# Performance work log

Hardware: AMD Instinct MI355X
Metric: run time of the kernel (lower is better)

The kernel has to match this reference:

```python
import jax, jax.numpy as jnp
import numpy as np

B, NAG = 8192, 16          # scenes, agents per scene
CIN, CH = 64, 128          # gnn_in_channels, gnn_out_channels
R2 = 8.0 * 8.0             # comm_range squared
BOX = 20.0                 # positions sampled uniformly in [0, BOX]^2


def _lin(k, fi, fo):
    k1, k2 = jax.random.split(k)
    s = 1.0 / np.sqrt(fi)
    W = jax.random.uniform(k1, (fi, fo), jnp.float32, -s, s)
    b = jax.random.uniform(k2, (fo,), jnp.float32, -s, s)
    return W, b


def setup_inputs() -> dict:
    key = jax.random.key(0)
    ks = jax.random.split(key, 10)
    x = jax.random.normal(ks[0], (B * NAG, CIN), jnp.float32)          # VAE mu per agent
    pos = jax.random.uniform(ks[1], (B, NAG, 2), jnp.float32) * BOX    # sensor xy positions
    W_rel1, b_rel1 = _lin(ks[2], CIN, CH)
    W_root1, _ = _lin(ks[3], CIN, CH)
    W_rel2, b_rel2 = _lin(ks[4], CH, CH)
    W_root2, _ = _lin(ks[5], CH, CH)
    Wh1, bh1 = _lin(ks[6], 2 * CH, 64)
    Wh2, bh2 = _lin(ks[7], 64, 32)
    Wh3, bh3 = _lin(ks[8], 32, 16)
    return dict(x=x, pos=pos, W_rel1=W_rel1, b_rel1=b_rel1, W_root1=W_root1,
                W_rel2=W_rel2, b_rel2=b_rel2, W_root2=W_root2,
                Wh1=Wh1, bh1=bh1, Wh2=Wh2, bh2=bh2, Wh3=Wh3, bh3=bh3)


def _graph_conv(h, adj, W_rel, b_rel, W_root):
    # PyG GraphConv (aggr='add'): out_i = W_rel @ sum_{j in N(i)} h_j + b_rel + W_root @ h_i
    nb = adj.shape[0]
    hb = h.reshape(nb, NAG, h.shape[-1])                 # [B, n, C]
    agg = jnp.einsum('bij,bjc->bic', adj, hb)            # neighbor sum within each scene
    return agg.reshape(h.shape[0], -1) @ W_rel + b_rel + h @ W_root


def reference(x, pos, W_rel1, b_rel1, W_root1, W_rel2, b_rel2, W_root2,
              Wh1, bh1, Wh2, bh2, Wh3, bh3):
    # radius_graph (batch-isolated, loop=False) as a per-scene dense mask
    diff = pos[:, :, None, :] - pos[:, None, :, :]       # [B, n, n, 2]
    d2 = jnp.sum(diff * diff, axis=-1)                   # [B, n, n]
    eye = jnp.eye(NAG, dtype=bool)
    adj = ((d2 <= R2) & ~eye).astype(x.dtype)            # [B, n, n]
    # Dropout(p=0.2) omitted (eval / deterministic reference).
    x1 = jax.nn.relu(_graph_conv(x, adj, W_rel1, b_rel1, W_root1))   # named 'x1' (inplace ReLU)
    x2 = jax.nn.relu(_graph_conv(x1, adj, W_rel2, b_rel2, W_root2))  # named 'x2' (inplace ReLU)
    h = jnp.concatenate([x1, x2], axis=-1)               # JumpingKnowledge('cat')
    h = jax.nn.relu(h @ Wh1 + bh1)
    h = jax.nn.relu(h @ Wh2 + bh2)
    out = h @ Wh3 + bh3                                  # [N, 16]
    return out.reshape(B, NAG, 16)
```

## Files before the change

### kernel.cpp

```cpp
#include <hip/hip_runtime.h>

#define NAG 16
#define SPB 4
#define NBLK 2048
#define R2f 64.0f

typedef unsigned short u16;
typedef __attribute__((ext_vector_type(8))) short short8;
typedef __attribute__((ext_vector_type(4))) float f32x4;

#define MFMA(a, b, c) __builtin_amdgcn_mfma_f32_16x16x32_bf16(a, b, c, 0, 0, 0)

#define OFF_B1 0
#define OFF_B2 16384
#define OFF_H1 49152
#define OFF_H2 65536
#define OFF_H3 67584
#define SWZ_UNITS 8512

__device__ __forceinline__ u16 f2b(float f) {
    unsigned u = __float_as_uint(f);
    unsigned r = u + 0x7FFFu + ((u >> 16) & 1u);
    return (u16)(r >> 16);
}

__global__ __launch_bounds__(256) void swizzle_w(
    const float* __restrict__ Wrel1, const float* __restrict__ Wroot1,
    const float* __restrict__ Wrel2, const float* __restrict__ Wroot2,
    const float* __restrict__ Wh1,  const float* __restrict__ Wh2,
    const float* __restrict__ Wh3,  u16* __restrict__ ws)
{
    const int u = blockIdx.x * 256 + threadIdx.x;
    if (u >= SWZ_UNITS) return;

    int v, T, N, ksplit;
    const float *W, *W2;
    u16* dst;
    if (u < 2048)      { v = u;        T = 8; N = 128; ksplit = 64;  W = Wroot1; W2 = Wrel1; dst = ws + OFF_B1 + v * 8; }
    else if (u < 6144) { v = u - 2048; T = 8; N = 128; ksplit = 128; W = Wroot2; W2 = Wrel2; dst = ws + OFF_B2 + v * 8; }
    else if (u < 8192) { v = u - 6144; T = 4; N = 64;  ksplit = 1 << 30; W = Wh1; W2 = Wh1; dst = ws + OFF_H1 + v * 8; }
    else if (u < 8448) { v = u - 8192; T = 2; N = 32;  ksplit = 1 << 30; W = Wh2; W2 = Wh2; dst = ws + OFF_H2 + v * 8; }
    else               { v = u - 8448; T = 1; N = 16;  ksplit = 1 << 30; W = Wh3; W2 = Wh3; dst = ws + OFF_H3 + v * 8; }

    const int lane = v & 63;
    const int t = (v >> 6) % T;
    const int s = (v >> 6) / T;
    const int n = t * 16 + (lane & 15);
    const int k0 = s * 32 + (lane >> 4) * 8;
    #pragma unroll
    for (int j = 0; j < 8; ++j) {
        const int k = k0 + j;
        const float val = (k < ksplit) ? W[k * N + n] : W2[(k - ksplit) * N + n];
        dst[j] = f2b(val);
    }
}

__device__ __forceinline__ short8 ldfrag(const u16* __restrict__ ws, int off,
                                         int T, int s, int tile, int lane) {
    return *(const short8*)(ws + off + (size_t)(((s * T + tile) * 64 + lane) * 8));
}

__device__ __forceinline__ short8 make_adjA(unsigned m, int q, int odd) {
    union { short8 v; unsigned u[4]; } r;
    const bool on = (q >> 1) == odd;
    const int base = (q & 1) * 8;
    #pragma unroll
    for (int jj = 0; jj < 4; ++jj) {
        const int k0 = base + 2 * jj;
        const unsigned lo = (on && ((m >> k0) & 1u)) ? 0x3F80u : 0u;
        const unsigned hi = (on && ((m >> (k0 + 1)) & 1u)) ? 0x3F80u : 0u;
        r.u[jj] = lo | (hi << 16);
    }
    return r.v;
}

__device__ __forceinline__ void relu_store4(u16* d, f32x4 a) {
    const unsigned p0 = (unsigned)f2b(fmaxf(a[0], 0.f)) | ((unsigned)f2b(fmaxf(a[1], 0.f)) << 16);
    const unsigned p1 = (unsigned)f2b(fmaxf(a[2], 0.f)) | ((unsigned)f2b(fmaxf(a[3], 0.f)) << 16);
    uint2 u; u.x = p0; u.y = p1;
    *(uint2*)d = u;
}

__global__ __launch_bounds__(256) void gnn_fused4(
    const float* __restrict__ x, const float* __restrict__ pos,
    const float* __restrict__ brel1, const float* __restrict__ brel2,
    const float* __restrict__ bh1,  const float* __restrict__ bh2,
    const float* __restrict__ bh3,
    const u16* __restrict__ ws, float* __restrict__ out)
{
    __shared__ __align__(16) u16 pool[39424];
    __shared__ unsigned mask[64];
    u16* const xcat = pool;
    u16* const xT   = pool + 8704;
    u16* const xc2  = pool + 13312;
    u16* const x1T  = pool + 30208;
    u16* const x2b  = pool;
    u16* const h1b  = pool + 8704;
    u16* const h2b  = pool + 30208;

    const int t = threadIdx.x;
    const int wv = t >> 6, lane = t & 63, ln = lane & 15, q = lane >> 4;
    const size_t sA = (size_t)blockIdx.x * SPB;

    {
        const int r = t >> 2;
        const int co = (t & 3) * 16;
        const float* src = x + (sA * 16 + r) * 64 + co;
        const float4 v0 = *(const float4*)(src);
        const float4 v1 = *(const float4*)(src + 4);
        const float4 v2 = *(const float4*)(src + 8);
        const float4 v3 = *(const float4*)(src + 12);
        u16 h[16];
        h[0] = f2b(v0.x); h[1] = f2b(v0.y); h[2]  = f2b(v0.z); h[3]  = f2b(v0.w);
        h[4] = f2b(v1.x); h[5] = f2b(v1.y); h[6]  = f2b(v1.z); h[7]  = f2b(v1.w);
        h[8] = f2b(v2.x); h[9] = f2b(v2.y); h[10] = f2b(v2.z); h[11] = f2b(v2.w);
        h[12]= f2b(v3.x); h[13]= f2b(v3.y); h[14] = f2b(v3.z); h[15] = f2b(v3.w);
        uint4 ua, ub;
        ua.x = (unsigned)h[0]  | ((unsigned)h[1]  << 16);
        ua.y = (unsigned)h[2]  | ((unsigned)h[3]  << 16);
        ua.z = (unsigned)h[4]  | ((unsigned)h[5]  << 16);
        ua.w = (unsigned)h[6]  | ((unsigned)h[7]  << 16);
        ub.x = (unsigned)h[8]  | ((unsigned)h[9]  << 16);
        ub.y = (unsigned)h[10] | ((unsigned)h[11] << 16);
        ub.z = (unsigned)h[12] | ((unsigned)h[13] << 16);
        ub.w = (unsigned)h[14] | ((unsigned)h[15] << 16);
        *(uint4*)&xcat[r * 136 + co]     = ua;
        *(uint4*)&xcat[r * 136 + co + 8] = ub;
        #pragma unroll
        for (int i = 0; i < 16; ++i)
            xT[(co + i) * 72 + r] = h[i];
    }
    if (t < 64) {
        const int g = t >> 4, a = t & 15;
        const float* pp = pos + (sA + g) * (NAG * 2);
        const float ax = pp[2 * a], ay = pp[2 * a + 1];
        unsigned m = 0;
        for (int j = 0; j < NAG; ++j) {
            const float dx = ax - pp[2 * j], dy = ay - pp[2 * j + 1];
            if (dx * dx + dy * dy <= R2f && j != a) m |= (1u << j);
        }
        mask[g * 16 + a] = m;
    }
    __syncthreads();

    {
        const int nt = wv;
        const short8 B0 = *(const short8*)&xT[(nt * 16 + ln) * 72 + q * 8];
        const short8 B1 = *(const short8*)&xT[(nt * 16 + ln) * 72 + 32 + q * 8];
        #pragma unroll
        for (int g = 0; g < 4; ++g) {
            const short8 A = make_adjA(mask[g * 16 + ln], q, g & 1);
            f32x4 acc = {0.f, 0.f, 0.f, 0.f};
            acc = MFMA(A, (g < 2) ? B0 : B1, acc);
            #pragma unroll
            for (int r = 0; r < 4; ++r)
                xcat[(g * 16 + q * 4 + r) * 136 + 64 + nt * 16 + ln] = f2b(acc[r]);
        }
    }
    __syncthreads();

    {
        const int n0 = 2 * wv, n1 = 2 * wv + 1;
        short8 Bf0[4], Bf1[4];
        #pragma unroll
        for (int s = 0; s < 4; ++s) {
            Bf0[s] = ldfrag(ws, OFF_B1, 8, s, n0, lane);
            Bf1[s] = ldfrag(ws, OFF_B1, 8, s, n1, lane);
        }
        const float b0 = brel1[n0 * 16 + ln], b1 = brel1[n1 * 16 + ln];
        #pragma unroll
        for (int m = 0; m < 4; ++m) {
            short8 Af[4];
            #pragma unroll
            for (int s = 0; s < 4; ++s)
                Af[s] = *(const short8*)&xcat[(m * 16 + ln) * 136 + s * 32 + q * 8];
            f32x4 a0 = {b0, b0, b0, b0}, a1 = {b1, b1, b1, b1};
            #pragma unroll
            for (int s = 0; s < 4; ++s) {
                a0 = MFMA(Af[s], Bf0[s], a0);
                a1 = MFMA(Af[s], Bf1[s], a1);
            }
            #pragma unroll
            for (int r = 0; r < 4; ++r) {
                const int row = m * 16 + q * 4 + r;
                xc2[row * 264 + n0 * 16 + ln] = f2b(fmaxf(a0[r], 0.f));
                xc2[row * 264 + n1 * 16 + ln] = f2b(fmaxf(a1[r], 0.f));
            }
            relu_store4(&x1T[(n0 * 16 + ln) * 72 + m * 16 + q * 4], a0);
            relu_store4(&x1T[(n1 * 16 + ln) * 72 + m * 16 + q * 4], a1);
        }
    }
    __syncthreads();

    {
        const int n0 = 2 * wv, n1 = 2 * wv + 1;
        short8 B00 = *(const short8*)&x1T[(n0 * 16 + ln) * 72 + q * 8];
        short8 B01 = *(const short8*)&x1T[(n0 * 16 + ln) * 72 + 32 + q * 8];
        short8 B10 = *(const short8*)&x1T[(n1 * 16 + ln) * 72 + q * 8];
        short8 B11 = *(const short8*)&x1T[(n1 * 16 + ln) * 72 + 32 + q * 8];
        #pragma unroll
        for (int g = 0; g < 4; ++g) {
            const short8 A = make_adjA(mask[g * 16 + ln], q, g & 1);
            f32x4 a0 = {0.f, 0.f, 0.f, 0.f}, a1 = a0;
            a0 = MFMA(A, (g < 2) ? B00 : B01, a0);
            a1 = MFMA(A, (g < 2) ? B10 : B11, a1);
            #pragma unroll
            for (int r = 0; r < 4; ++r) {
                const int row = g * 16 + q * 4 + r;
                xc2[row * 264 + 128 + n0 * 16 + ln] = f2b(a0[r]);
                xc2[row * 264 + 128 + n1 * 16 + ln] = f2b(a1[r]);
            }
        }
    }
    __syncthreads();

    {
        const int n0 = 2 * wv, n1 = 2 * wv + 1;
        short8 Bf0[8], Bf1[8];
        #pragma unroll
        for (int s = 0; s < 8; ++s) {
            Bf0[s] = ldfrag(ws, OFF_B2, 8, s, n0, lane);
            Bf1[s] = ldfrag(ws, OFF_B2, 8, s, n1, lane);
        }
        const float b0 = brel2[n0 * 16 + ln], b1 = brel2[n1 * 16 + ln];
        #pragma unroll
        for (int m = 0; m < 4; ++m) {
            short8 Af[8];
            #pragma unroll
            for (int s = 0; s < 8; ++s)
                Af[s] = *(const short8*)&xc2[(m * 16 + ln) * 264 + s * 32 + q * 8];
            f32x4 a0 = {b0, b0, b0, b0}, a1 = {b1, b1, b1, b1};
            f32x4 c0 = {0.f, 0.f, 0.f, 0.f}, c1 = c0;
            #pragma unroll
            for (int s = 0; s < 4; ++s) {
                a0 = MFMA(Af[s], Bf0[s], a0);
                a1 = MFMA(Af[s], Bf1[s], a1);
                c0 = MFMA(Af[s + 4], Bf0[s + 4], c0);
                c1 = MFMA(Af[s + 4], Bf1[s + 4], c1);
            }
            #pragma unroll
            for (int r = 0; r < 4; ++r) {
                const int row = m * 16 + q * 4 + r;
                x2b[row * 136 + n0 * 16 + ln] = f2b(fmaxf(a0[r] + c0[r], 0.f));
                x2b[row * 136 + n1 * 16 + ln] = f2b(fmaxf(a1[r] + c1[r], 0.f));
            }
        }
    }
    __syncthreads();

    {
        const int nt = wv;
        short8 Bf[8];
        #pragma unroll
        for (int s = 0; s < 8; ++s)
            Bf[s] = ldfrag(ws, OFF_H1, 4, s, nt, lane);
        const float b = bh1[nt * 16 + ln];
        #pragma unroll
        for (int m = 0; m < 4; ++m) {
            short8 Af[8];
            #pragma unroll
            for (int s = 0; s < 4; ++s)
                Af[s] = *(const short8*)&xc2[(m * 16 + ln) * 264 + s * 32 + q * 8];
            #pragma unroll
            for (int s = 0; s < 4; ++s)
                Af[s + 4] = *(const short8*)&x2b[(m * 16 + ln) * 136 + s * 32 + q * 8];
            f32x4 a = {b, b, b, b}, c = {0.f, 0.f, 0.f, 0.f};
            #pragma unroll
            for (int s = 0; s < 4; ++s) {
                a = MFMA(Af[s], Bf[s], a);
                c = MFMA(Af[s + 4], Bf[s + 4], c);
            }
            #pragma unroll
            for (int r = 0; r < 4; ++r)
                h1b[(m * 16 + q * 4 + r) * 72 + nt * 16 + ln] = f2b(fmaxf(a[r] + c[r], 0.f));
        }
    }
    __syncthreads();

    {
        const int nt = wv & 1;
        const int m0 = (wv >> 1) * 2;
        short8 Bf[2];
        Bf[0] = ldfrag(ws, OFF_H2, 2, 0, nt, lane);
        Bf[1] = ldfrag(ws, OFF_H2, 2, 1, nt, lane);
        const float b = bh2[nt * 16 + ln];
        #pragma unroll
        for (int mi = 0; mi < 2; ++mi) {
            const int m = m0 + mi;
            const short8 A0 = *(const short8*)&h1b[(m * 16 + ln) * 72 + q * 8];
            const short8 A1 = *(const short8*)&h1b[(m * 16 + ln) * 72 + 32 + q * 8];
            f32x4 a = {b, b, b, b};
            a = MFMA(A0, Bf[0], a);
            a = MFMA(A1, Bf[1], a);
            #pragma unroll
            for (int r = 0; r < 4; ++r)
                h2b[(m * 16 + q * 4 + r) * 40 + nt * 16 + ln] = f2b(fmaxf(a[r], 0.f));
        }
    }
    __syncthreads();

    {
        const int m = wv;
        const short8 A = *(const short8*)&h2b[(m * 16 + ln) * 40 + q * 8];
        const short8 B = ldfrag(ws, OFF_H3, 1, 0, 0, lane);
        const float b = bh3[ln];
        f32x4 a = {b, b, b, b};
        a = MFMA(A, B, a);
        float* o = out + (sA * 16 + m * 16) * 16;
        #pragma unroll
        for (int r = 0; r < 4; ++r)
            o[(q * 4 + r) * 16 + ln] = a[r];
    }
}

extern "C" void kernel_launch(void* const* d_in, const int* in_sizes, int n_in,
                              void* d_out, int out_size, void* d_ws, size_t ws_size,
                              hipStream_t stream) {
    const float* x      = (const float*)d_in[0];
    const float* pos    = (const float*)d_in[1];
    const float* Wrel1  = (const float*)d_in[2];
    const float* brel1  = (const float*)d_in[3];
    const float* Wroot1 = (const float*)d_in[4];
    const float* Wrel2  = (const float*)d_in[5];
    const float* brel2  = (const float*)d_in[6];
    const float* Wroot2 = (const float*)d_in[7];
    const float* Wh1    = (const float*)d_in[8];
    const float* bh1    = (const float*)d_in[9];
    const float* Wh2    = (const float*)d_in[10];
    const float* bh2    = (const float*)d_in[11];
    const float* Wh3    = (const float*)d_in[12];
    const float* bh3    = (const float*)d_in[13];
    u16* ws = (u16*)d_ws;

    swizzle_w<<<(SWZ_UNITS + 255) / 256, 256, 0, stream>>>(
        Wrel1, Wroot1, Wrel2, Wroot2, Wh1, Wh2, Wh3, ws);
    gnn_fused4<<<NBLK, 256, 0, stream>>>(
        x, pos, brel1, brel2, bh1, bh2, bh3, ws, (float*)d_out);
}
```

Measured before the change: 135.6 us.

## Reassociate GraphConv as adj@(h@W_rel) and shrink shared memory footprint

Each GraphConv layer now computes h@W_rel first, stores the result transposed in LDS, and then applies the adjacency MFMA to that projected result. The root term and the bias are accumulated into the same accumulator. This drops the separate aggregation pass, the concatenated xcat/xc2 buffers and one barrier, and the last two head layers are merged into one stage, so LDS use falls from about 79KB to about 53KB, which may raise occupancy. It also replaces round-to-nearest-even bf16 conversion with a cheaper round-half-up, which can change results slightly, and the adjacency fragments are built once and reused by both layers.

```diff
diff --git a/kernel.cpp b/kernel.cpp
--- a/kernel.cpp
+++ b/kernel.cpp
@@ -22,6 +22,13 @@
     unsigned u = __float_as_uint(f);
     unsigned r = u + 0x7FFFu + ((u >> 16) & 1u);
     return (u16)(r >> 16);
+}
+__device__ __forceinline__ unsigned rb(float f) {
+    return (__float_as_uint(f) + 0x8000u) >> 16;
+}
+__device__ __forceinline__ unsigned pk2(float a, float b) {
+    return ((__float_as_uint(a) + 0x8000u) >> 16) |
+           ((__float_as_uint(b) + 0x8000u) & 0xFFFF0000u);
 }
 
 __global__ __launch_bounds__(256) void swizzle_w(
@@ -32,7 +39,6 @@
 {
     const int u = blockIdx.x * 256 + threadIdx.x;
     if (u >= SWZ_UNITS) return;
-
     int v, T, N, ksplit;
     const float *W, *W2;
     u16* dst;
@@ -41,7 +47,6 @@
     else if (u < 8192) { v = u - 6144; T = 4; N = 64;  ksplit = 1 << 30; W = Wh1; W2 = Wh1; dst = ws + OFF_H1 + v * 8; }
     else if (u < 8448) { v = u - 8192; T = 2; N = 32;  ksplit = 1 << 30; W = Wh2; W2 = Wh2; dst = ws + OFF_H2 + v * 8; }
     else               { v = u - 8448; T = 1; N = 16;  ksplit = 1 << 30; W = Wh3; W2 = Wh3; dst = ws + OFF_H3 + v * 8; }
-
     const int lane = v & 63;
     const int t = (v >> 6) % T;
     const int s = (v >> 6) / T;
@@ -74,61 +79,39 @@
     return r.v;
 }
 
-__device__ __forceinline__ void relu_store4(u16* d, f32x4 a) {
-    const unsigned p0 = (unsigned)f2b(fmaxf(a[0], 0.f)) | ((unsigned)f2b(fmaxf(a[1], 0.f)) << 16);
-    const unsigned p1 = (unsigned)f2b(fmaxf(a[2], 0.f)) | ((unsigned)f2b(fmaxf(a[3], 0.f)) << 16);
-    uint2 u; u.x = p0; u.y = p1;
-    *(uint2*)d = u;
-}
-
-__global__ __launch_bounds__(256) void gnn_fused4(
+__global__ __launch_bounds__(256) void gnn_fused5(
     const float* __restrict__ x, const float* __restrict__ pos,
     const float* __restrict__ brel1, const float* __restrict__ brel2,
     const float* __restrict__ bh1,  const float* __restrict__ bh2,
     const float* __restrict__ bh3,
     const u16* __restrict__ ws, float* __restrict__ out)
 {
-    __shared__ __align__(16) u16 pool[39424];
+    __shared__ __align__(16) u16 pool[26624];
     __shared__ unsigned mask[64];
-    u16* const xcat = pool;
-    u16* const xT   = pool + 8704;
-    u16* const xc2  = pool + 13312;
-    u16* const x1T  = pool + 30208;
-    u16* const x2b  = pool;
-    u16* const h1b  = pool + 8704;
-    u16* const h2b  = pool + 30208;
+    u16* const xb  = pool;
+    u16* const yT  = pool + 8704;
+    u16* const x1b = pool + 17920;
 
     const int t = threadIdx.x;
     const int wv = t >> 6, lane = t & 63, ln = lane & 15, q = lane >> 4;
+    const int c0 = 32 * wv;
+    const int n0 = 2 * wv, n1 = 2 * wv + 1;
     const size_t sA = (size_t)blockIdx.x * SPB;
 
     {
-        const int r = t >> 2;
-        const int co = (t & 3) * 16;
+        const int r = t >> 2, co = (t & 3) * 16;
         const float* src = x + (sA * 16 + r) * 64 + co;
         const float4 v0 = *(const float4*)(src);
         const float4 v1 = *(const float4*)(src + 4);
         const float4 v2 = *(const float4*)(src + 8);
         const float4 v3 = *(const float4*)(src + 12);
-        u16 h[16];
-        h[0] = f2b(v0.x); h[1] = f2b(v0.y); h[2]  = f2b(v0.z); h[3]  = f2b(v0.w);
-        h[4] = f2b(v1.x); h[5] = f2b(v1.y); h[6]  = f2b(v1.z); h[7]  = f2b(v1.w);
-        h[8] = f2b(v2.x); h[9] = f2b(v2.y); h[10] = f2b(v2.z); h[11] = f2b(v2.w);
-        h[12]= f2b(v3.x); h[13]= f2b(v3.y); h[14] = f2b(v3.z); h[15] = f2b(v3.w);
         uint4 ua, ub;
-        ua.x = (unsigned)h[0]  | ((unsigned)h[1]  << 16);
-        ua.y = (unsigned)h[2]  | ((unsigned)h[3]  << 16);
-        ua.z = (unsigned)h[4]  | ((unsigned)h[5]  << 16);
-        ua.w = (unsigned)h[6]  | ((unsigned)h[7]  << 16);
-        ub.x = (unsigned)h[8]  | ((unsigned)h[9]  << 16);
-        ub.y = (unsigned)h[10] | ((unsigned)h[11] << 16);
-        ub.z = (unsigned)h[12] | ((unsigned)h[13] << 16);
-        ub.w = (unsigned)h[14] | ((unsigned)h[15] << 16);
-        *(uint4*)&xcat[r * 136 + co]     = ua;
-        *(uint4*)&xcat[r * 136 + co + 8] = ub;
-        #pragma unroll
-        for (int i = 0; i < 16; ++i)
-            xT[(co + i) * 72 + r] = h[i];
+        ua.x = pk2(v0.x, v0.y); ua.y = pk2(v0.z, v0.w);
+        ua.z = pk2(v1.x, v1.y); ua.w = pk2(v1.z, v1.w);
+        ub.x = pk2(v2.x, v2.y); ub.y = pk2(v2.z, v2.w);
+        ub.z = pk2(v3.x, v3.y); ub.w = pk2(v3.z, v3.w);
+        *(uint4*)&xb[r * 136 + co]     = ua;
+        *(uint4*)&xb[r * 136 + co + 8] = ub;
     }
     if (t < 64) {
         const int g = t >> 4, a = t & 15;
@@ -143,173 +126,160 @@
     }
     __syncthreads();
 
-    {
-        const int nt = wv;
-        const short8 B0 = *(const short8*)&xT[(nt * 16 + ln) * 72 + q * 8];
-        const short8 B1 = *(const short8*)&xT[(nt * 16 + ln) * 72 + 32 + q * 8];
+    short8 adjA[4];
+    #pragma unroll
+    for (int g = 0; g < 4; ++g) adjA[g] = make_adjA(mask[g * 16 + ln], q, g & 1);
+
+    {
+        short8 Brl[2][2], Bro[2][2], Af[4][2];
+        #pragma unroll
+        for (int s = 0; s < 2; ++s) {
+            Brl[s][0] = ldfrag(ws, OFF_B1, 8, s + 2, n0, lane);
+            Brl[s][1] = ldfrag(ws, OFF_B1, 8, s + 2, n1, lane);
+        }
+        #pragma unroll
+        for (int m = 0; m < 4; ++m) {
+            Af[m][0] = *(const short8*)&xb[(m * 16 + ln) * 136 + q * 8];
+            Af[m][1] = *(const short8*)&xb[(m * 16 + ln) * 136 + 32 + q * 8];
+            f32x4 a0 = {0.f, 0.f, 0.f, 0.f}, a1 = a0;
+            a0 = MFMA(Af[m][0], Brl[0][0], a0); a0 = MFMA(Af[m][1], Brl[1][0], a0);
+            a1 = MFMA(Af[m][0], Brl[0][1], a1); a1 = MFMA(Af[m][1], Brl[1][1], a1);
+            uint2 u0; u0.x = pk2(a0[0], a0[1]); u0.y = pk2(a0[2], a0[3]);
+            uint2 u1; u1.x = pk2(a1[0], a1[1]); u1.y = pk2(a1[2], a1[3]);
+            *(uint2*)&yT[(c0 + ln) * 72 + m * 16 + q * 4]      = u0;
+            *(uint2*)&yT[(c0 + 16 + ln) * 72 + m * 16 + q * 4] = u1;
+        }
+        short8 By[2][2];
+        #pragma unroll
+        for (int w = 0; w < 2; ++w) {
+            By[w][0] = *(const short8*)&yT[(c0 + ln) * 72 + w * 32 + q * 8];
+            By[w][1] = *(const short8*)&yT[(c0 + 16 + ln) * 72 + w * 32 + q * 8];
+        }
+        #pragma unroll
+        for (int s = 0; s < 2; ++s) {
+            Bro[s][0] = ldfrag(ws, OFF_B1, 8, s, n0, lane);
+            Bro[s][1] = ldfrag(ws, OFF_B1, 8, s, n1, lane);
+        }
+        const float b0 = brel1[c0 + ln], b1 = brel1[c0 + 16 + ln];
         #pragma unroll
         for (int g = 0; g < 4; ++g) {
-            const short8 A = make_adjA(mask[g * 16 + ln], q, g & 1);
-            f32x4 acc = {0.f, 0.f, 0.f, 0.f};
-            acc = MFMA(A, (g < 2) ? B0 : B1, acc);
-            #pragma unroll
-            for (int r = 0; r < 4; ++r)
-                xcat[(g * 16 + q * 4 + r) * 136 + 64 + nt * 16 + ln] = f2b(acc[r]);
-        }
-    }
-    __syncthreads();
-
-    {
-        const int n0 = 2 * wv, n1 = 2 * wv + 1;
-        short8 Bf0[4], Bf1[4];
-        #pragma unroll
-        for (int s = 0; s < 4; ++s) {
-            Bf0[s] = ldfrag(ws, OFF_B1, 8, s, n0, lane);
-            Bf1[s] = ldfrag(ws, OFF_B1, 8, s, n1, lane);
-        }
-        const float b0 = brel1[n0 * 16 + ln], b1 = brel1[n1 * 16 + ln];
-        #pragma unroll
-        for (int m = 0; m < 4; ++m) {
-            short8 Af[4];
-            #pragma unroll
-            for (int s = 0; s < 4; ++s)
-                Af[s] = *(const short8*)&xcat[(m * 16 + ln) * 136 + s * 32 + q * 8];
             f32x4 a0 = {b0, b0, b0, b0}, a1 = {b1, b1, b1, b1};
-            #pragma unroll
-            for (int s = 0; s < 4; ++s) {
-                a0 = MFMA(Af[s], Bf0[s], a0);
-                a1 = MFMA(Af[s], Bf1[s], a1);
-            }
-            #pragma unroll
-            for (int r = 0; r < 4; ++r) {
-                const int row = m * 16 + q * 4 + r;
-                xc2[row * 264 + n0 * 16 + ln] = f2b(fmaxf(a0[r], 0.f));
-                xc2[row * 264 + n1 * 16 + ln] = f2b(fmaxf(a1[r], 0.f));
-            }
-            relu_store4(&x1T[(n0 * 16 + ln) * 72 + m * 16 + q * 4], a0);
-            relu_store4(&x1T[(n1 * 16 + ln) * 72 + m * 16 + q * 4], a1);
-        }
-    }
-    __syncthreads();
-
-    {
-        const int n0 = 2 * wv, n1 = 2 * wv + 1;
-        short8 B00 = *(const short8*)&x1T[(n0 * 16 + ln) * 72 + q * 8];
-        short8 B01 = *(const short8*)&x1T[(n0 * 16 + ln) * 72 + 32 + q * 8];
-        short8 B10 = *(const short8*)&x1T[(n1 * 16 + ln) * 72 + q * 8];
-        short8 B11 = *(const short8*)&x1T[(n1 * 16 + ln) * 72 + 32 + q * 8];
-        #pragma unroll
-        for (int g = 0; g < 4; ++g) {
-            const short8 A = make_adjA(mask[g * 16 + ln], q, g & 1);
-            f32x4 a0 = {0.f, 0.f, 0.f, 0.f}, a1 = a0;
-            a0 = MFMA(A, (g < 2) ? B00 : B01, a0);
-            a1 = MFMA(A, (g < 2) ? B10 : B11, a1);
+            a0 = MFMA(Af[g][0], Bro[0][0], a0); a0 = MFMA(Af[g][1], Bro[1][0], a0);
+            a1 = MFMA(Af[g][0], Bro[0][1], a1); a1 = MFMA(Af[g][1], Bro[1][1], a1);
+            a0 = MFMA(adjA[g], By[g >> 1][0], a0);
+            a1 = MFMA(adjA[g], By[g >> 1][1], a1);
             #pragma unroll
             for (int r = 0; r < 4; ++r) {
                 const int row = g * 16 + q * 4 + r;
-                xc2[row * 264 + 128 + n0 * 16 + ln] = f2b(a0[r]);
-                xc2[row * 264 + 128 + n1 * 16 + ln] = f2b(a1[r]);
+                x1b[row * 136 + c0 + ln]      = (u16)rb(fmaxf(a0[r], 0.f));
+                x1b[row * 136 + c0 + 16 + ln] = (u16)rb(fmaxf(a1[r], 0.f));
             }
         }
     }
     __syncthreads();
 
     {
-        const int n0 = 2 * wv, n1 = 2 * wv + 1;
-        short8 Bf0[8], Bf1[8];
-        #pragma unroll
-        for (int s = 0; s < 8; ++s) {
-            Bf0[s] = ldfrag(ws, OFF_B2, 8, s, n0, lane);
-            Bf1[s] = ldfrag(ws, OFF_B2, 8, s, n1, lane);
-        }
-        const float b0 = brel2[n0 * 16 + ln], b1 = brel2[n1 * 16 + ln];
+        short8 Brl[4][2];
+        #pragma unroll
+        for (int s = 0; s < 4; ++s) {
+            Brl[s][0] = ldfrag(ws, OFF_B2, 8, s + 4, n0, lane);
+            Brl[s][1] = ldfrag(ws, OFF_B2, 8, s + 4, n1, lane);
+        }
         #pragma unroll
         for (int m = 0; m < 4; ++m) {
-            short8 Af[8];
-            #pragma unroll
-            for (int s = 0; s < 8; ++s)
-                Af[s] = *(const short8*)&xc2[(m * 16 + ln) * 264 + s * 32 + q * 8];
+            f32x4 a0 = {0.f, 0.f, 0.f, 0.f}, a1 = a0;
+            #pragma unroll
+            for (int s = 0; s < 4; ++s) {
+                const short8 A = *(const short8*)&x1b[(m * 16 + ln) * 136 + s * 32 + q * 8];
+                a0 = MFMA(A, Brl[s][0], a0);
+                a1 = MFMA(A, Brl[s][1], a1);
+            }
+            uint2 u0; u0.x = pk2(a0[0], a0[1]); u0.y = pk2(a0[2], a0[3]);
+            uint2 u1; u1.x = pk2(a1[0], a1[1]); u1.y = pk2(a1[2], a1[3]);
+            *(uint2*)&yT[(c0 + ln) * 72 + m * 16 + q * 4]      = u0;
+            *(uint2*)&yT[(c0 + 16 + ln) * 72 + m * 16 + q * 4] = u1;
+        }
+        short8 By[2][2];
+        #pragma unroll
+        for (int w = 0; w < 2; ++w) {
+            By[w][0] = *(const short8*)&yT[(c0 + ln) * 72 + w * 32 + q * 8];
+            By[w][1] = *(const short8*)&yT[(c0 + 16 + ln) * 72 + w * 32 + q * 8];
+        }
+        short8 Bro[4][2];
+        #pragma unroll
+        for (int s = 0; s < 4; ++s) {
+            Bro[s][0] = ldfrag(ws, OFF_B2, 8, s, n0, lane);
+            Bro[s][1] = ldfrag(ws, OFF_B2, 8, s, n1, lane);
+        }
+        const float b0 = brel2[c0 + ln], b1 = brel2[c0 + 16 + ln];
+        #pragma unroll
+        for (int g = 0; g < 4; ++g) {
             f32x4 a0 = {b0, b0, b0, b0}, a1 = {b1, b1, b1, b1};
-            f32x4 c0 = {0.f, 0.f, 0.f, 0.f}, c1 = c0;
             #pragma unroll
             for (int s = 0; s < 4; ++s) {
-                a0 = MFMA(Af[s], Bf0[s], a0);
-                a1 = MFMA(Af[s], Bf1[s], a1);
-                c0 = MFMA(Af[s + 4], Bf0[s + 4], c0);
-                c1 = MFMA(Af[s + 4], Bf1[s + 4], c1);
-            }
+                const short8 A = *(const short8*)&x1b[(g * 16 + ln) * 136 + s * 32 + q * 8];
+                a0 = MFMA(A, Bro[s][0], a0);
+                a1 = MFMA(A, Bro[s][1], a1);
+            }
+            a0 = MFMA(adjA[g], By[g >> 1][0], a0);
+            a1 = MFMA(adjA[g], By[g >> 1][1], a1);
             #pragma unroll
             for (int r = 0; r < 4; ++r) {
-                const int row = m * 16 + q * 4 + r;
-                x2b[row * 136 + n0 * 16 + ln] = f2b(fmaxf(a0[r] + c0[r], 0.f));
-                x2b[row * 136 + n1 * 16 + ln] = f2b(fmaxf(a1[r] + c1[r], 0.f));
+                const int row = g * 16 + q * 4 + r;
+                xb[row * 136 + c0 + ln]      = (u16)rb(fmaxf(a0[r], 0.f));
+                xb[row * 136 + c0 + 16 + ln] = (u16)rb(fmaxf(a1[r], 0.f));
             }
         }
     }
     __syncthreads();
 
     {
-        const int nt = wv;
         short8 Bf[8];
         #pragma unroll
-        for (int s = 0; s < 8; ++s)
-            Bf[s] = ldfrag(ws, OFF_H1, 4, s, nt, lane);
-        const float b = bh1[nt * 16 + ln];
+        for (int s = 0; s < 8; ++s) Bf[s] = ldfrag(ws, OFF_H1, 4, s, wv, lane);
+        const float b = bh1[wv * 16 + ln];
         #pragma unroll
         for (int m = 0; m < 4; ++m) {
-            short8 Af[8];
-            #pragma unroll
-            for (int s = 0; s < 4; ++s)
-                Af[s] = *(const short8*)&xc2[(m * 16 + ln) * 264 + s * 32 + q * 8];
-            #pragma unroll
-            for (int s = 0; s < 4; ++s)
-                Af[s + 4] = *(const short8*)&x2b[(m * 16 + ln) * 136 + s * 32 + q * 8];
             f32x4 a = {b, b, b, b}, c = {0.f, 0.f, 0.f, 0.f};
             #pragma unroll
             for (int s = 0; s < 4; ++s) {
-                a = MFMA(Af[s], Bf[s], a);
-                c = MFMA(Af[s + 4], Bf[s + 4], c);
+                const short8 A1 = *(const short8*)&x1b[(m * 16 + ln) * 136 + s * 32 + q * 8];
+                const short8 A2 = *(const short8*)&xb[(m * 16 + ln) * 136 + s * 32 + q * 8];
+                a = MFMA(A1, Bf[s], a);
+                c = MFMA(A2, Bf[s + 4], c);
             }
             #pragma unroll
             for (int r = 0; r < 4; ++r)
-                h1b[(m * 16 + q * 4 + r) * 72 + nt * 16 + ln] = f2b(fmaxf(a[r] + c[r], 0.f));
+                yT[(m * 16 + q * 4 + r) * 72 + wv * 16 + ln] = (u16)rb(fmaxf(a[r] + c[r], 0.f));
         }
     }
     __syncthreads();
 
     {
-        const int nt = wv & 1;
-        const int m0 = (wv >> 1) * 2;
-        short8 Bf[2];
-        Bf[0] = ldfrag(ws, OFF_H2, 2, 0, nt, lane);
-        Bf[1] = ldfrag(ws, OFF_H2, 2, 1, nt, lane);
-        const float b = bh2[nt * 16 + ln];
-        #pragma unroll
-        for (int mi = 0; mi < 2; ++mi) {
-            const int m = m0 + mi;
-            const short8 A0 = *(const short8*)&h1b[(m * 16 + ln) * 72 + q * 8];
-            const short8 A1 = *(const short8*)&h1b[(m * 16 + ln) * 72 + 32 + q * 8];
+        const u16* h1b = yT;
+        u16* h2b = x1b;
+        const short8 A0 = *(const short8*)&h1b[(wv * 16 + ln) * 72 + q * 8];
+        const short8 A1 = *(const short8*)&h1b[(wv * 16 + ln) * 72 + 32 + q * 8];
+        #pragma unroll
+        for (int nt = 0; nt < 2; ++nt) {
+            const short8 B0 = ldfrag(ws, OFF_H2, 2, 0, nt, lane);
+            const short8 B1 = ldfrag(ws, OFF_H2, 2, 1, nt, lane);
+            const float b = bh2[nt * 16 + ln];
             f32x4 a = {b, b, b, b};
-            a = MFMA(A0, Bf[0], a);
-            a = MFMA(A1, Bf[1], a);
+            a = MFMA(A0, B0, a);
+            a = MFMA(A1, B1, a);
             #pragma unroll
             for (int r = 0; r < 4; ++r)
-                h2b[(m * 16 + q * 4 + r) * 40 + nt * 16 + ln] = f2b(fmaxf(a[r], 0.f));
-        }
-    }
-    __syncthreads();
-
-    {
-        const int m = wv;
-        const short8 A = *(const short8*)&h2b[(m * 16 + ln) * 40 + q * 8];
+                h2b[(wv * 16 + q * 4 + r) * 40 + nt * 16 + ln] = (u16)rb(fmaxf(a[r], 0.f));
+        }
+        const short8 A = *(const short8*)&h2b[(wv * 16 + ln) * 40 + q * 8];
         const short8 B = ldfrag(ws, OFF_H3, 1, 0, 0, lane);
         const float b = bh3[ln];
         f32x4 a = {b, b, b, b};
         a = MFMA(A, B, a);
-        float* o = out + (sA * 16 + m * 16) * 16;
         #pragma unroll
         for (int r = 0; r < 4; ++r)
-            o[(q * 4 + r) * 16 + ln] = a[r];
+            out[(sA * 16 + wv * 16 + q * 4 + r) * 16 + ln] = a[r];
     }
 }
 
@@ -334,6 +304,6 @@
 
     swizzle_w<<<(SWZ_UNITS + 255) / 256, 256, 0, stream>>>(
         Wrel1, Wroot1, Wrel2, Wroot2, Wh1, Wh2, Wh3, ws);
-    gnn_fused4<<<NBLK, 256, 0, stream>>>(
+    gnn_fused5<<<NBLK, 256, 0, stream>>>(
         x, pos, brel1, brel2, bh1, bh2, bh3, ws, (float*)d_out);
 }
```

After: 125.0 us. -7.8%, faster.
